# Kernel tuning notes

Hardware: AMD Instinct MI355X
Metric: run time of the kernel (lower is better)

## Reference

```python
import jax, jax.numpy as jnp
import numpy as np

B, C, H, W = 8, 64, 64, 64
CQK = C // 8

def setup_inputs() -> dict:
    key = jax.random.key(0)
    ks = jax.random.split(key, 8)
    s = 0.05
    return {
        "X": jax.random.normal(ks[0], (B, C, H, W), dtype=jnp.float32),
        "Wq": jax.random.normal(ks[1], (CQK, C), dtype=jnp.float32) * s,
        "bq": jax.random.normal(ks[2], (CQK,), dtype=jnp.float32) * s,
        "Wk": jax.random.normal(ks[3], (CQK, C), dtype=jnp.float32) * s,
        "bk": jax.random.normal(ks[4], (CQK,), dtype=jnp.float32) * s,
        "Wv": jax.random.normal(ks[5], (C, C), dtype=jnp.float32) * s,
        "bv": jax.random.normal(ks[6], (C,), dtype=jnp.float32) * s,
        "gamma": jax.random.normal(ks[7], (1,), dtype=jnp.float32) * 0.5,
    }

def reference(X, Wq, bq, Wk, bk, Wv, bv, gamma):
    b, c, h, w = X.shape
    n = h * w
    Xf = X.reshape(b, c, n)  # [B, C, N]
    # 1x1 convs == per-pixel linear over channels
    q = jnp.einsum('oc,bcn->bno', Wq, Xf) + bq            # [B, N, Cqk]
    k = jnp.einsum('oc,bcn->bon', Wk, Xf) + bk[:, None]    # [B, Cqk, N]
    v = jnp.einsum('oc,bcn->bon', Wv, Xf) + bv[:, None]    # [B, C, N]
    energy = jnp.einsum('bnd,bdm->bnm', q, k)              # [B, N, N] (no scale, as in source)
    attention = jax.nn.softmax(energy, axis=-1)
    out = jnp.einsum('bcn,bmn->bcm', v, attention)         # value @ attention^T
    out = out.reshape(b, c, h, w)
    return X + out * gamma[0]
```

## Files before the change

### kernel.cpp

```cpp
#include <hip/hip_runtime.h>
#include <hip/hip_bf16.h>

#define BB 8
#define CC 64
#define NN 4096
#define LOG2E 1.44269504088896340736f

typedef short bf16x8 __attribute__((ext_vector_type(8)));
typedef float f32x16 __attribute__((ext_vector_type(16)));
typedef unsigned int uint4v __attribute__((ext_vector_type(4)));

__device__ __forceinline__ unsigned cvt_pk_bf16(float lo, float hi) {
    unsigned r;
    asm("v_cvt_pk_bf16_f32 %0, %1, %2" : "=v"(r) : "v"(lo), "v"(hi));
    return r;
}

__device__ __forceinline__ float fast_exp2(float x) {
#if __has_builtin(__builtin_amdgcn_exp2f)
    return __builtin_amdgcn_exp2f(x);
#else
    return __builtin_exp2f(x);
#endif
}


__global__ __launch_bounds__(256) void qkv_kernel(
    const float* __restrict__ X,
    const float* __restrict__ Wq, const float* __restrict__ bq,
    const float* __restrict__ Wk, const float* __restrict__ bk,
    const float* __restrict__ Wv, const float* __restrict__ bv,
    unsigned short* __restrict__ qw, unsigned short* __restrict__ kfrag,
    unsigned short* __restrict__ vfrag)
{
    __shared__ float wbuf[64 * 16];
    __shared__ float bsh[16];
    __shared__ short vsh[16][264];

    const int t = threadIdx.x;
    const int grp = blockIdx.x % 5;
    const int tile = blockIdx.x / 5;
    const int b = tile >> 4;
    const int nb = (tile & 15) << 8;
    const int n = nb + t;

    if (grp == 0) {
        for (int i = t; i < 512; i += 256) {
            int o = i >> 6, c = i & 63;
            wbuf[c * 16 + o]     = Wq[i];
            wbuf[c * 16 + 8 + o] = Wk[i];
        }
        if (t < 8) { bsh[t] = bq[t]; bsh[8 + t] = bk[t]; }
    } else {
        const int cbase = (grp - 1) * 16;
        for (int i = t; i < 1024; i += 256) {
            int o = i >> 6, c = i & 63;
            wbuf[c * 16 + o] = Wv[(cbase + o) * 64 + c];
        }
        if (t < 16) bsh[t] = bv[cbase + t];
    }
    __syncthreads();

    float a[16];
    #pragma unroll
    for (int j = 0; j < 16; j++) a[j] = bsh[j];

    const float* xp = X + (size_t)b * CC * NN + n;
    for (int c = 0; c < 64; c++) {
        float xc = xp[(size_t)c * NN];
        const float4* w4 = (const float4*)&wbuf[c * 16];
        float4 w0 = w4[0], w1 = w4[1], w2 = w4[2], w3 = w4[3];
        a[0]  += w0.x * xc; a[1]  += w0.y * xc; a[2]  += w0.z * xc; a[3]  += w0.w * xc;
        a[4]  += w1.x * xc; a[5]  += w1.y * xc; a[6]  += w1.z * xc; a[7]  += w1.w * xc;
        a[8]  += w2.x * xc; a[9]  += w2.y * xc; a[10] += w2.z * xc; a[11] += w2.w * xc;
        a[12] += w3.x * xc; a[13] += w3.y * xc; a[14] += w3.z * xc; a[15] += w3.w * xc;
    }

    if (grp == 0) {
        alignas(16) __hip_bfloat16 qb8[8], kb8[8];
        #pragma unroll
        for (int d = 0; d < 8; d++) {
            qb8[d] = __float2bfloat16(a[d] * LOG2E);
            kb8[d] = __float2bfloat16(a[8 + d]);
        }
        const size_t g = (size_t)b * NN + n;
        *(int4*)(qw + g * 8) = *(const int4*)qb8;
        size_t kf = ((size_t)b * 128 + (n >> 5)) * 512;
        *(int4*)(kfrag + kf + (size_t)(n & 31) * 8) = *(const int4*)kb8;
        *(int4*)(kfrag + kf + (size_t)(32 + (n & 31)) * 8) = make_int4(0, 0, 0, 0);
    } else {
        const int cbase = (grp - 1) * 16;
        const int qb0 = cbase & 31, ct = cbase >> 5;
        #pragma unroll
        for (int j = 0; j < 16; j++)
            vsh[j][t] = __builtin_bit_cast(short, __float2bfloat16(a[j]));
        __syncthreads();
        #pragma unroll
        for (int rr = 0; rr < 2; ++rr) {
            int r = 2 * t + rr;
            int qq = r & 15, hh = (r >> 4) & 1, gg = (r >> 5) & 3, tau = r >> 7;
            int n0 = tau * 64 + gg * 16 + hh * 8;
            int4 val = *(const int4*)&vsh[qq][n0];
            int gtile = (nb >> 6) + tau;
            size_t dst = ((size_t)(b * 64 + gtile)) * 4096
                       + (size_t)(gg * 2 + ct) * 512
                       + (size_t)(32 * hh + qb0 + qq) * 8;
            *(int4*)(vfrag + dst) = val;
        }
    }
}

template<int KS, bool FUSE>
__global__ __launch_bounds__(256, 2) void attn_kernel(
    const unsigned short* __restrict__ qw,
    const unsigned short* __restrict__ kfrag,
    const unsigned short* __restrict__ vfrag,
    unsigned short* __restrict__ pout, float* __restrict__ pl,
    const float* __restrict__ X, const float* __restrict__ gamma,
    float* __restrict__ out)
{
    const int t = threadIdx.x;
    const int w = t >> 6, lane = t & 63;
    const int h = lane >> 5, q = lane & 31;

    const int nwg = gridDim.x;
    const int cpx = nwg >> 3;
    const int bid = (blockIdx.x & 7) * cpx + (blockIdx.x >> 3);

    const int qtile = bid & 15;
    const int b = (bid >> 4) & 7;
    const int ks = bid >> 7;

    const int qbase = qtile * 256 + w * 64;

    bf16x8 qfA = {}, qfB = {};
    if (h == 0) {
        qfA = *(const bf16x8*)(qw + ((size_t)b * NN + qbase + q) * 8);
        qfB = *(const bf16x8*)(qw + ((size_t)b * NN + qbase + 32 + q) * 8);
    }

    f32x16 accA0 = {}, accA1 = {}, accB0 = {}, accB1 = {};
    float lsumA = 0.f, lsumB = 0.f;

    const int NT = NN / KS / 64;
    const int tile0 = ks * NT;
    const unsigned short* kb = kfrag + (size_t)b * 65536;
    const unsigned short* vb = vfrag + (size_t)b * 262144;

    for (int it = 0; it < NT; ++it) {
        const int gt = tile0 + it;
        const unsigned short* kp = kb + (size_t)gt * 1024 + (size_t)lane * 8;
        bf16x8 kf0 = *(const bf16x8*)kp;
        bf16x8 kf1 = *(const bf16x8*)(kp + 512);

        f32x16 sA0 = __builtin_amdgcn_mfma_f32_32x32x16_bf16(kf0, qfA, (f32x16){}, 0, 0, 0);
        f32x16 sA1 = __builtin_amdgcn_mfma_f32_32x32x16_bf16(kf1, qfA, (f32x16){}, 0, 0, 0);
        f32x16 sB0 = __builtin_amdgcn_mfma_f32_32x32x16_bf16(kf0, qfB, (f32x16){}, 0, 0, 0);
        f32x16 sB1 = __builtin_amdgcn_mfma_f32_32x32x16_bf16(kf1, qfB, (f32x16){}, 0, 0, 0);

        unsigned pkA[16], pkB[16];
        {
            float pa[16], pb2[16];
            #pragma unroll
            for (int r = 0; r < 16; ++r) { pa[r] = fast_exp2(sA0[r]); pb2[r] = fast_exp2(sA1[r]); }
            float t0 = 0.f, t1 = 0.f, t2 = 0.f, t3 = 0.f;
            #pragma unroll
            for (int r = 0; r < 4; ++r) {
                t0 += pa[r]; t1 += pa[4 + r]; t2 += pa[8 + r]; t3 += pa[12 + r];
                t0 += pb2[r]; t1 += pb2[4 + r]; t2 += pb2[8 + r]; t3 += pb2[12 + r];
            }
            lsumA += (t0 + t1) + (t2 + t3);
            #pragma unroll
            for (int j = 0; j < 8; ++j) {
                pkA[j]     = cvt_pk_bf16(pa[2 * j], pa[2 * j + 1]);
                pkA[8 + j] = cvt_pk_bf16(pb2[2 * j], pb2[2 * j + 1]);
            }
            #pragma unroll
            for (int r = 0; r < 16; ++r) { pa[r] = fast_exp2(sB0[r]); pb2[r] = fast_exp2(sB1[r]); }
            t0 = t1 = t2 = t3 = 0.f;
            #pragma unroll
            for (int r = 0; r < 4; ++r) {
                t0 += pa[r]; t1 += pa[4 + r]; t2 += pa[8 + r]; t3 += pa[12 + r];
                t0 += pb2[r]; t1 += pb2[4 + r]; t2 += pb2[8 + r]; t3 += pb2[12 + r];
            }
            lsumB += (t0 + t1) + (t2 + t3);
            #pragma unroll
            for (int j = 0; j < 8; ++j) {
                pkB[j]     = cvt_pk_bf16(pa[2 * j], pa[2 * j + 1]);
                pkB[8 + j] = cvt_pk_bf16(pb2[2 * j], pb2[2 * j + 1]);
            }
        }

        const unsigned short* vp = vb + (size_t)gt * 4096 + (size_t)lane * 8;
        __builtin_amdgcn_s_setprio(1);
        #pragma unroll
        for (int g = 0; g < 4; ++g) {
            const unsigned* pga = &pkA[4 * g];
            auto ra = __builtin_amdgcn_permlane32_swap(pga[2], pga[0], false, false);
            auto rb = __builtin_amdgcn_permlane32_swap(pga[3], pga[1], false, false);
            uint4v bua = { ra[1], rb[1], ra[0], rb[0] };
            bf16x8 pfA = __builtin_bit_cast(bf16x8, bua);
            const unsigned* pgb = &pkB[4 * g];
            auto rc = __builtin_amdgcn_permlane32_swap(pgb[2], pgb[0], false, false);
            auto rd = __builtin_amdgcn_permlane32_swap(pgb[3], pgb[1], false, false);
            uint4v bub = { rc[1], rd[1], rc[0], rd[0] };
            bf16x8 pfB = __builtin_bit_cast(bf16x8, bub);

            bf16x8 v0 = *(const bf16x8*)(vp + (size_t)(g * 2) * 512);
            bf16x8 v1 = *(const bf16x8*)(vp + (size_t)(g * 2 + 1) * 512);
            accA0 = __builtin_amdgcn_mfma_f32_32x32x16_bf16(v0, pfA, accA0, 0, 0, 0);
            accA1 = __builtin_amdgcn_mfma_f32_32x32x16_bf16(v1, pfA, accA1, 0, 0, 0);
            accB0 = __builtin_amdgcn_mfma_f32_32x32x16_bf16(v0, pfB, accB0, 0, 0, 0);
            accB1 = __builtin_amdgcn_mfma_f32_32x32x16_bf16(v1, pfB, accB1, 0, 0, 0);
        }
        __builtin_amdgcn_s_setprio(0);
    }

    auto rsA = __builtin_amdgcn_permlane32_swap(__builtin_bit_cast(unsigned, lsumA),
                                                __builtin_bit_cast(unsigned, lsumA), false, false);
    float ltotA = __builtin_bit_cast(float, rsA[0]) + __builtin_bit_cast(float, rsA[1]);
    auto rsB = __builtin_amdgcn_permlane32_swap(__builtin_bit_cast(unsigned, lsumB),
                                                __builtin_bit_cast(unsigned, lsumB), false, false);
    float ltotB = __builtin_bit_cast(float, rsB[0]) + __builtin_bit_cast(float, rsB[1]);

    const float gm = FUSE ? gamma[0] : 0.f;

    #pragma unroll
    for (int sub = 0; sub < 2; ++sub) {
        const int n = qbase + sub * 32 + q;
        const float ltot = sub ? ltotB : ltotA;
        const f32x16& a0 = sub ? accB0 : accA0;
        const f32x16& a1 = sub ? accB1 : accA1;
        if (FUSE) {
            const float inv = 1.f / ltot;
            #pragma unroll
            for (int ct = 0; ct < 2; ++ct) {
                const f32x16& a = ct ? a1 : a0;
                #pragma unroll
                for (int r = 0; r < 16; ++r) {
                    int c = ct * 32 + (r & 3) + 8 * (r >> 2) + 4 * h;
                    size_t idx = ((size_t)(b * CC + c)) * NN + n;
                    out[idx] = X[idx] + gm * a[r] * inv;
                }
            }
        } else {
            unsigned short* po = pout + (size_t)ks * BB * CC * NN;
            #pragma unroll
            for (int ct = 0; ct < 2; ++ct) {
                const f32x16& a = ct ? a1 : a0;
                #pragma unroll
                for (int r = 0; r < 16; ++r) {
                    int c = ct * 32 + (r & 3) + 8 * (r >> 2) + 4 * h;
                    po[((size_t)(b * CC + c)) * NN + n] =
                        __builtin_bit_cast(unsigned short, __float2bfloat16(a[r]));
                }
            }
            if (h == 0) pl[((size_t)(ks * BB + b)) * NN + n] = ltot;
        }
    }
}

template<int KS>
__global__ __launch_bounds__(256) void combine_kernel(
    const unsigned short* __restrict__ pout, const float* __restrict__ pl,
    const float* __restrict__ X, const float* __restrict__ gamma,
    float* __restrict__ out)
{
    const int idx = blockIdx.x * 256 + threadIdx.x;
    const int n4 = idx & 1023;
    const int c  = (idx >> 10) & 63;
    const int b  = idx >> 16;
    const int n0 = n4 * 4;
    const float gm = gamma[0];
    const size_t base = ((size_t)(b * CC + c)) * NN + n0;

    float4 s = make_float4(0.f, 0.f, 0.f, 0.f);
    float4 L = make_float4(0.f, 0.f, 0.f, 0.f);
    #pragma unroll
    for (int ks = 0; ks < KS; ++ks) {
        ushort4 sv = *(const ushort4*)(pout + (size_t)ks * BB * CC * NN + base);
        float4 lv = *(const float4*)(pl + ((size_t)(ks * BB + b)) * NN + n0);
        s.x += __bfloat162float(__builtin_bit_cast(__hip_bfloat16, sv.x));
        s.y += __bfloat162float(__builtin_bit_cast(__hip_bfloat16, sv.y));
        s.z += __bfloat162float(__builtin_bit_cast(__hip_bfloat16, sv.z));
        s.w += __bfloat162float(__builtin_bit_cast(__hip_bfloat16, sv.w));
        L.x += lv.x; L.y += lv.y; L.z += lv.z; L.w += lv.w;
    }
    float4 x = *(const float4*)(X + base);
    float4 o;
    o.x = x.x + gm * s.x / L.x;
    o.y = x.y + gm * s.y / L.y;
    o.z = x.z + gm * s.z / L.z;
    o.w = x.w + gm * s.w / L.w;
    *(float4*)(out + base) = o;
}

extern "C" void kernel_launch(void* const* d_in, const int* in_sizes, int n_in,
                              void* d_out, int out_size, void* d_ws, size_t ws_size,
                              hipStream_t stream) {
    const float* X  = (const float*)d_in[0];
    const float* Wq = (const float*)d_in[1];
    const float* bq = (const float*)d_in[2];
    const float* Wk = (const float*)d_in[3];
    const float* bk = (const float*)d_in[4];
    const float* Wv = (const float*)d_in[5];
    const float* bv = (const float*)d_in[6];
    const float* gm = (const float*)d_in[7];
    float* out = (float*)d_out;

    unsigned short* qw    = (unsigned short*)d_ws;
    unsigned short* kfrag = qw + (size_t)BB * NN * 8;
    unsigned short* vfrag = kfrag + (size_t)BB * 128 * 512;
    unsigned short* pout  = vfrag + (size_t)BB * 64 * 4096;
    float* pl = (float*)(pout + (size_t)4 * BB * CC * NN);

    const size_t qkv_bytes = ((size_t)BB * NN * 8 + (size_t)BB * 128 * 512
                            + (size_t)BB * 64 * 4096) * 2;
    const size_t need4 = qkv_bytes + (size_t)4 * BB * CC * NN * 2 + (size_t)4 * BB * NN * 4;
    const size_t need2 = qkv_bytes + (size_t)2 * BB * CC * NN * 2 + (size_t)2 * BB * NN * 4;

    qkv_kernel<<<dim3(640), dim3(256), 0, stream>>>(X, Wq, bq, Wk, bk, Wv, bv, qw, kfrag, vfrag);

    if (ws_size >= need4) {
        attn_kernel<4, false><<<dim3(512), dim3(256), 0, stream>>>(
            qw, kfrag, vfrag, pout, pl, X, gm, out);
        combine_kernel<4><<<dim3((BB * CC * NN / 4) / 256), dim3(256), 0, stream>>>(
            pout, pl, X, gm, out);
    } else if (ws_size >= need2) {
        float* pl2 = (float*)(pout + (size_t)2 * BB * CC * NN);
        attn_kernel<2, false><<<dim3(256), dim3(256), 0, stream>>>(
            qw, kfrag, vfrag, pout, pl2, X, gm, out);
        combine_kernel<2><<<dim3((BB * CC * NN / 4) / 256), dim3(256), 0, stream>>>(
            pout, pl2, X, gm, out);
    } else {
        attn_kernel<1, true><<<dim3(128), dim3(256), 0, stream>>>(
            qw, kfrag, vfrag, nullptr, nullptr, X, gm, out);
    }
}
```

Baseline: 58.49 us.

## Prefetch next K tile and split attention inner loop into two half-tile phases

```diff
diff --git a/kernel.cpp b/kernel.cpp
--- a/kernel.cpp
+++ b/kernel.cpp
@@ -143,77 +143,87 @@
     float lsumA = 0.f, lsumB = 0.f;
 
     const int NT = NN / KS / 64;
-    const int tile0 = ks * NT;
-    const unsigned short* kb = kfrag + (size_t)b * 65536;
-    const unsigned short* vb = vfrag + (size_t)b * 262144;
-
-    for (int it = 0; it < NT; ++it) {
-        const int gt = tile0 + it;
-        const unsigned short* kp = kb + (size_t)gt * 1024 + (size_t)lane * 8;
-        bf16x8 kf0 = *(const bf16x8*)kp;
-        bf16x8 kf1 = *(const bf16x8*)(kp + 512);
-
-        f32x16 sA0 = __builtin_amdgcn_mfma_f32_32x32x16_bf16(kf0, qfA, (f32x16){}, 0, 0, 0);
-        f32x16 sA1 = __builtin_amdgcn_mfma_f32_32x32x16_bf16(kf1, qfA, (f32x16){}, 0, 0, 0);
-        f32x16 sB0 = __builtin_amdgcn_mfma_f32_32x32x16_bf16(kf0, qfB, (f32x16){}, 0, 0, 0);
-        f32x16 sB1 = __builtin_amdgcn_mfma_f32_32x32x16_bf16(kf1, qfB, (f32x16){}, 0, 0, 0);
-
-        unsigned pkA[16], pkB[16];
+    const unsigned short* kb = kfrag + (size_t)b * 65536
+                             + (size_t)ks * NT * 1024 + (size_t)lane * 8;
+    const unsigned short* vbp = vfrag + (size_t)b * 262144
+                              + (size_t)ks * NT * 4096 + (size_t)lane * 8;
+
+    auto phase = [&](const f32x16& sA, const f32x16& sB,
+                     bf16x8 va, bf16x8 vb2, bf16x8 vc, bf16x8 vd) {
+        float pa[16], pb[16];
+        #pragma unroll
+        for (int r = 0; r < 16; ++r) { pa[r] = fast_exp2(sA[r]); pb[r] = fast_exp2(sB[r]); }
         {
-            float pa[16], pb2[16];
+            float a0 = 0.f, a1 = 0.f, b0 = 0.f, b1 = 0.f;
             #pragma unroll
-            for (int r = 0; r < 16; ++r) { pa[r] = fast_exp2(sA0[r]); pb2[r] = fast_exp2(sA1[r]); }
-            float t0 = 0.f, t1 = 0.f, t2 = 0.f, t3 = 0.f;
-            #pragma unroll
-            for (int r = 0; r < 4; ++r) {
-                t0 += pa[r]; t1 += pa[4 + r]; t2 += pa[8 + r]; t3 += pa[12 + r];
-                t0 += pb2[r]; t1 += pb2[4 + r]; t2 += pb2[8 + r]; t3 += pb2[12 + r];
+            for (int r = 0; r < 8; ++r) {
+                a0 += pa[r]; a1 += pa[8 + r];
+                b0 += pb[r]; b1 += pb[8 + r];
             }
-            lsumA += (t0 + t1) + (t2 + t3);
-            #pragma unroll
-            for (int j = 0; j < 8; ++j) {
-                pkA[j]     = cvt_pk_bf16(pa[2 * j], pa[2 * j + 1]);
-                pkA[8 + j] = cvt_pk_bf16(pb2[2 * j], pb2[2 * j + 1]);
-            }
-            #pragma unroll
-            for (int r = 0; r < 16; ++r) { pa[r] = fast_exp2(sB0[r]); pb2[r] = fast_exp2(sB1[r]); }
-            t0 = t1 = t2 = t3 = 0.f;
-            #pragma unroll
-            for (int r = 0; r < 4; ++r) {
-                t0 += pa[r]; t1 += pa[4 + r]; t2 += pa[8 + r]; t3 += pa[12 + r];
-                t0 += pb2[r]; t1 += pb2[4 + r]; t2 += pb2[8 + r]; t3 += pb2[12 + r];
-            }
-            lsumB += (t0 + t1) + (t2 + t3);
-            #pragma unroll
-            for (int j = 0; j < 8; ++j) {
-                pkB[j]     = cvt_pk_bf16(pa[2 * j], pa[2 * j + 1]);
-                pkB[8 + j] = cvt_pk_bf16(pb2[2 * j], pb2[2 * j + 1]);
-            }
-        }
-
-        const unsigned short* vp = vb + (size_t)gt * 4096 + (size_t)lane * 8;
+            lsumA += a0 + a1;
+            lsumB += b0 + b1;
+        }
+        unsigned ka[8], kb2[8];
+        #pragma unroll
+        for (int j = 0; j < 8; ++j) {
+            ka[j]  = cvt_pk_bf16(pa[2 * j], pa[2 * j + 1]);
+            kb2[j] = cvt_pk_bf16(pb[2 * j], pb[2 * j + 1]);
+        }
         __builtin_amdgcn_s_setprio(1);
         #pragma unroll
-        for (int g = 0; g < 4; ++g) {
-            const unsigned* pga = &pkA[4 * g];
+        for (int g2 = 0; g2 < 2; ++g2) {
+            const unsigned* pga = &ka[4 * g2];
             auto ra = __builtin_amdgcn_permlane32_swap(pga[2], pga[0], false, false);
             auto rb = __builtin_amdgcn_permlane32_swap(pga[3], pga[1], false, false);
             uint4v bua = { ra[1], rb[1], ra[0], rb[0] };
             bf16x8 pfA = __builtin_bit_cast(bf16x8, bua);
-            const unsigned* pgb = &pkB[4 * g];
+            const unsigned* pgb = &kb2[4 * g2];
             auto rc = __builtin_amdgcn_permlane32_swap(pgb[2], pgb[0], false, false);
             auto rd = __builtin_amdgcn_permlane32_swap(pgb[3], pgb[1], false, false);
             uint4v bub = { rc[1], rd[1], rc[0], rd[0] };
             bf16x8 pfB = __builtin_bit_cast(bf16x8, bub);
 
-            bf16x8 v0 = *(const bf16x8*)(vp + (size_t)(g * 2) * 512);
-            bf16x8 v1 = *(const bf16x8*)(vp + (size_t)(g * 2 + 1) * 512);
-            accA0 = __builtin_amdgcn_mfma_f32_32x32x16_bf16(v0, pfA, accA0, 0, 0, 0);
-            accA1 = __builtin_amdgcn_mfma_f32_32x32x16_bf16(v1, pfA, accA1, 0, 0, 0);
-            accB0 = __builtin_amdgcn_mfma_f32_32x32x16_bf16(v0, pfB, accB0, 0, 0, 0);
-            accB1 = __builtin_amdgcn_mfma_f32_32x32x16_bf16(v1, pfB, accB1, 0, 0, 0);
+            bf16x8 vx = g2 ? vc : va;
+            bf16x8 vy = g2 ? vd : vb2;
+            accA0 = __builtin_amdgcn_mfma_f32_32x32x16_bf16(vx, pfA, accA0, 0, 0, 0);
+            accA1 = __builtin_amdgcn_mfma_f32_32x32x16_bf16(vy, pfA, accA1, 0, 0, 0);
+            accB0 = __builtin_amdgcn_mfma_f32_32x32x16_bf16(vx, pfB, accB0, 0, 0, 0);
+            accB1 = __builtin_amdgcn_mfma_f32_32x32x16_bf16(vy, pfB, accB1, 0, 0, 0);
         }
         __builtin_amdgcn_s_setprio(0);
+    };
+
+    bf16x8 kc0 = *(const bf16x8*)kb;
+    bf16x8 kc1 = *(const bf16x8*)(kb + 512);
+
+    for (int it = 0; it < NT; ++it) {
+        const unsigned short* vp = vbp + (size_t)it * 4096;
+        bf16x8 v0 = *(const bf16x8*)(vp);
+        bf16x8 v1 = *(const bf16x8*)(vp + 512);
+        bf16x8 v2 = *(const bf16x8*)(vp + 1024);
+        bf16x8 v3 = *(const bf16x8*)(vp + 1536);
+        bf16x8 v4 = *(const bf16x8*)(vp + 2048);
+        bf16x8 v5 = *(const bf16x8*)(vp + 2560);
+        bf16x8 v6 = *(const bf16x8*)(vp + 3072);
+        bf16x8 v7 = *(const bf16x8*)(vp + 3584);
+
+        const int nit = (it + 1 < NT) ? it + 1 : it;
+        const unsigned short* knp = kb + (size_t)nit * 1024;
+        bf16x8 kn0 = *(const bf16x8*)knp;
+        bf16x8 kn1 = *(const bf16x8*)(knp + 512);
+
+        {
+            f32x16 sA = __builtin_amdgcn_mfma_f32_32x32x16_bf16(kc0, qfA, (f32x16){}, 0, 0, 0);
+            f32x16 sB = __builtin_amdgcn_mfma_f32_32x32x16_bf16(kc0, qfB, (f32x16){}, 0, 0, 0);
+            phase(sA, sB, v0, v1, v2, v3);
+        }
+        {
+            f32x16 sA = __builtin_amdgcn_mfma_f32_32x32x16_bf16(kc1, qfA, (f32x16){}, 0, 0, 0);
+            f32x16 sB = __builtin_amdgcn_mfma_f32_32x32x16_bf16(kc1, qfB, (f32x16){}, 0, 0, 0);
+            phase(sA, sB, v4, v5, v6, v7);
+        }
+        kc0 = kn0;
+        kc1 = kn1;
     }
 
     auto rsA = __builtin_amdgcn_permlane32_swap(__builtin_bit_cast(unsigned, lsumA),
```

Measured after the change: 51.51 us. -11.9%, faster.
